# Kernel optimization log

Hardware: AMD Instinct MI355X
Metric: run time of the kernel (lower is better)

The kernel has to match this reference:

```python
import jax, jax.numpy as jnp
import numpy as np

D = 128
N_DRUG = 100000
N_PROT = 50000
E_DD, E_DP, E_PD = 800000, 600000, 600000
EPS = 1e-5


def setup_inputs() -> dict:
    key = jax.random.key(0)
    ks = jax.random.split(key, 19)
    f32 = jnp.float32
    return {
        "x_drug": jax.random.normal(ks[0], (N_DRUG, D), f32),
        "x_prot": jax.random.normal(ks[1], (N_PROT, D), f32),
        "Wagg_dd": jax.random.normal(ks[2], (D, D), f32) * 0.05,
        "Wagg_dp": jax.random.normal(ks[3], (D, D), f32) * 0.05,
        "Wagg_pd": jax.random.normal(ks[4], (D, D), f32) * 0.05,
        "W_drug": jax.random.normal(ks[5], (D, 2 * D), f32) * 0.05,
        "b_drug": jax.random.normal(ks[6], (D,), f32) * 0.01,
        "W_prot": jax.random.normal(ks[7], (D, 2 * D), f32) * 0.05,
        "b_prot": jax.random.normal(ks[8], (D,), f32) * 0.01,
        "g_drug": jnp.ones((D,), f32),
        "be_drug": jnp.zeros((D,), f32),
        "g_prot": jnp.ones((D,), f32),
        "be_prot": jnp.zeros((D,), f32),
        "ei_dd_src": jax.random.randint(ks[9], (E_DD,), 0, N_DRUG, jnp.int64 if jax.config.jax_enable_x64 else jnp.int32),
        "ei_dd_dst": jax.random.randint(ks[10], (E_DD,), 0, N_DRUG),
        "ei_dp_src": jax.random.randint(ks[11], (E_DP,), 0, N_DRUG),
        "ei_dp_dst": jax.random.randint(ks[12], (E_DP,), 0, N_PROT),
        "ei_pd_src": jax.random.randint(ks[13], (E_PD,), 0, N_PROT),
        "ei_pd_dst": jax.random.randint(ks[14], (E_PD,), 0, N_DRUG),
    }


def _rel_agg(x_src, W_agg, src_idx, dst_idx, n_dst):
    # gather -> per-relation Linear (no bias) + ReLU -> scatter-mean
    h = jax.nn.relu(x_src[src_idx] @ W_agg.T)            # [E, D]
    s = jax.ops.segment_sum(h, dst_idx, num_segments=n_dst)
    c = jax.ops.segment_sum(jnp.ones((src_idx.shape[0],), h.dtype), dst_idx, num_segments=n_dst)
    return s / jnp.maximum(c, 1.0)[:, None]


def _layernorm(x, g, b):
    mu = jnp.mean(x, axis=-1, keepdims=True)
    var = jnp.mean(jnp.square(x - mu), axis=-1, keepdims=True)
    return (x - mu) * jax.lax.rsqrt(var + EPS) * g + b


def _node_update(h_self, h_agg, W, b, g, be):
    h = jax.nn.relu(jnp.concatenate([h_self, h_agg], axis=-1) @ W.T + b)
    return _layernorm(h + h_self, g, be)  # dropout is identity in eval


def reference(x_drug, x_prot, Wagg_dd, Wagg_dp, Wagg_pd, W_drug, b_drug,
              W_prot, b_prot, g_drug, be_drug, g_prot, be_prot,
              ei_dd_src, ei_dd_dst, ei_dp_src, ei_dp_dst, ei_pd_src, ei_pd_dst):
    agg_dd = _rel_agg(x_drug, Wagg_dd, ei_dd_src, ei_dd_dst, N_DRUG)
    agg_pd = _rel_agg(x_prot, Wagg_pd, ei_pd_src, ei_pd_dst, N_DRUG)
    agg_drug = (agg_dd + agg_pd) * 0.5                   # mean over relations into 'drug'
    agg_prot = _rel_agg(x_drug, Wagg_dp, ei_dp_src, ei_dp_dst, N_PROT)
    out_drug = _node_update(x_drug, agg_drug, W_drug, b_drug, g_drug, be_drug)
    out_prot = _node_update(x_prot, agg_prot, W_prot, b_prot, g_prot, be_prot)
    # pack the per-type outputs into one array [N_DRUG + N_PROT, D]
    return jnp.concatenate([out_drug, out_prot], axis=0)
```

## Files before the change

kernel.cpp:

```cpp
#include <hip/hip_runtime.h>

#define D 128
#define ND 100000
#define NP 50000
#define NE_DD 800000
#define NE_DP 600000
#define NE_PD 600000
#define NE_TOT 2000000

#define NTOT 250000
#define NBC 490
#define NC 250880
#define CHUNKA 4096
#define NBLKA 489
#define CHUNKIT 16
#define SEGCAP 8192

#define TF_BD 1563
#define TF_BP 391
#define NU_BD 782
#define NU_BP 391

typedef __bf16 bf16;
typedef __attribute__((ext_vector_type(8))) __bf16 bf16x8;
typedef __attribute__((ext_vector_type(2))) __bf16 bf16x2;
typedef __attribute__((ext_vector_type(4))) float f32x4;
typedef __attribute__((ext_vector_type(2))) float f32x2;

#define OFF_WDD   0UL
#define OFF_WDP   32768UL
#define OFF_WPD   65536UL
#define OFF_WDRUG 98304UL
#define OFF_WPROT 163840UL
#define OFF_YDD   229376UL
#define OFF_YDP   (OFF_YDD + 25600000UL)
#define OFF_YPD   (OFF_YDP + 25600000UL)
#define OFF_AGGD  (OFF_YPD + 12800000UL)
#define OFF_AGGP  (OFF_AGGD + 25600000UL)
#define OFF_BCNT  (OFF_AGGP + 12800000UL)
#define OFF_GCUR  (OFF_BCNT + 2048UL)
#define OFF_CBASE (OFF_GCUR + 2048UL)
#define OFF_RP    (OFF_CBASE + 2048UL)
#define OFF_PAIRS (OFF_RP + 1003520UL)
#define OFF_POOL  (OFF_PAIRS + 16000000UL)

__device__ __forceinline__ unsigned enc1(float f)
{
    unsigned t = __float_as_uint(f * 0x1p-120f);
    t = (t + 0x80000u) >> 20;
    return t > 0x7Eu ? 0x7Eu : t;
}
__device__ __forceinline__ unsigned enc4(float a, float b, float c, float d)
{
    return enc1(a) | (enc1(b) << 8) | (enc1(c) << 16) | (enc1(d) << 24);
}

__global__ __launch_bounds__(256) void prep_kernel(
    const float* __restrict__ w0, const float* __restrict__ w1,
    const float* __restrict__ w2, const float* __restrict__ w3,
    const float* __restrict__ w4,
    bf16* __restrict__ o0, bf16* __restrict__ o1, bf16* __restrict__ o2,
    bf16* __restrict__ o3, bf16* __restrict__ o4,
    const int* __restrict__ dd_dst, const int* __restrict__ pd_dst,
    const int* __restrict__ dp_dst, int* __restrict__ bcnt)
{
    int m = blockIdx.y;
    int t = threadIdx.x;
    if (m == 5) {
        __shared__ int h[NBC];
        for (int i = t; i < NBC; i += 256) h[i] = 0;
        __syncthreads();
        for (int e = blockIdx.x * 256 + t; e < NE_TOT; e += 128 * 256) {
            int didx;
            if (e < NE_DD) didx = dd_dst[e];
            else if (e < NE_DD + NE_PD) didx = ND + pd_dst[e - NE_DD];
            else didx = 2 * ND + dp_dst[e - NE_DD - NE_PD];
            atomicAdd(&h[didx >> 9], 1);
        }
        __syncthreads();
        for (int i = t; i < NBC; i += 256)
            if (h[i]) atomicAdd(&bcnt[i], h[i]);
        return;
    }
    int i = blockIdx.x * 256 + t;
    const float* src; bf16* dst; int n; bool perm;
    switch (m) {
        case 0: src = w0; dst = o0; n = D * D; perm = false; break;
        case 1: src = w1; dst = o1; n = D * D; perm = false; break;
        case 2: src = w2; dst = o2; n = D * D; perm = false; break;
        case 3: src = w3; dst = o3; n = D * 2 * D; perm = true; break;
        default: src = w4; dst = o4; n = D * 2 * D; perm = true; break;
    }
    if (i < n) {
        int si = i;
        if (perm) {
            int col = i & 255;
            if (col >= 128) {
                int p = col - 128;
                si = (i & ~255) | (128 + (p & 7) * 16 + (p >> 3));
            }
        }
        dst[i] = (bf16)src[si];
    }
}

__global__ __launch_bounds__(256) void scan_kernel(
    const int* __restrict__ bcnt, int* __restrict__ cbase, int* __restrict__ gcur)
{
    __shared__ int ps[256];
    int t = threadIdx.x;
    int i0 = 2 * t, i1 = 2 * t + 1;
    int c0 = (i0 < NBC) ? bcnt[i0] : 0;
    int c1 = (i1 < NBC) ? bcnt[i1] : 0;
    ps[t] = c0 + c1;
    __syncthreads();
#pragma unroll
    for (int off = 1; off < 256; off <<= 1) {
        int add = (t >= off) ? ps[t - off] : 0;
        __syncthreads();
        ps[t] += add;
        __syncthreads();
    }
    int excl = ps[t] - (c0 + c1);
    if (i0 <= NBC) cbase[i0] = excl;
    if (i0 < NBC) gcur[i0] = excl;
    if (i1 < NBC) { cbase[i1] = excl + c0; gcur[i1] = excl + c0; }
}

__device__ __forceinline__ bf16x8 load_a_f32(const float* __restrict__ xr)
{
    float4 f0 = *(const float4*)xr;
    float4 f1 = *(const float4*)(xr + 4);
    bf16x8 a;
    a[0] = (bf16)f0.x; a[1] = (bf16)f0.y; a[2] = (bf16)f0.z; a[3] = (bf16)f0.w;
    a[4] = (bf16)f1.x; a[5] = (bf16)f1.y; a[6] = (bf16)f1.z; a[7] = (bf16)f1.w;
    return a;
}

__device__ __forceinline__ void transform_drug(
    const float* __restrict__ x, const bf16* __restrict__ W1,
    const bf16* __restrict__ W2, unsigned char* __restrict__ y1,
    unsigned char* __restrict__ y2, int blk)
{
    int lane = threadIdx.x & 63;
    int wave = threadIdx.x >> 6;
    int q = lane >> 4, c = lane & 15;
    int mb = blk * 64 + wave * 16;

    f32x4 acc1[8], acc2[8];
#pragma unroll
    for (int nt = 0; nt < 8; nt++) { acc1[nt] = 0; acc2[nt] = 0; }

    int rowA = min(mb + c, ND - 1);
#pragma unroll
    for (int kb = 0; kb < 4; kb++) {
        int k = kb * 32 + q * 8;
        bf16x8 a = load_a_f32(x + (long)rowA * D + k);
#pragma unroll
        for (int nt = 0; nt < 8; nt++) {
            bf16x8 b1 = *(const bf16x8*)(W1 + (nt * 16 + c) * D + k);
            bf16x8 b2 = *(const bf16x8*)(W2 + (nt * 16 + c) * D + k);
            acc1[nt] = __builtin_amdgcn_mfma_f32_16x16x32_bf16(a, b1, acc1[nt], 0, 0, 0);
            acc2[nt] = __builtin_amdgcn_mfma_f32_16x16x32_bf16(a, b2, acc2[nt], 0, 0, 0);
        }
    }
#pragma unroll
    for (int r = 0; r < 4; r++) {
        int row = mb + q * 4 + r;
        if (row < ND) {
            float v1[8], v2[8];
#pragma unroll
            for (int nt = 0; nt < 8; nt++) {
                v1[nt] = fmaxf(acc1[nt][r], 0.f);
                v2[nt] = fmaxf(acc2[nt][r], 0.f);
            }
            uint2 p1, p2;
            p1.x = enc4(v1[0], v1[1], v1[2], v1[3]);
            p1.y = enc4(v1[4], v1[5], v1[6], v1[7]);
            p2.x = enc4(v2[0], v2[1], v2[2], v2[3]);
            p2.y = enc4(v2[4], v2[5], v2[6], v2[7]);
            *(uint2*)(y1 + (long)row * D + c * 8) = p1;
            *(uint2*)(y2 + (long)row * D + c * 8) = p2;
        }
    }
}

__device__ __forceinline__ void transform_prot(
    const float* __restrict__ x, const bf16* __restrict__ W1,
    unsigned char* __restrict__ y1, int blk)
{
    int lane = threadIdx.x & 63;
    int wave = threadIdx.x >> 6;
    int q = lane >> 4, c = lane & 15;
    int mb = blk * 128 + wave * 32;

    f32x4 acc[2][8];
#pragma unroll
    for (int mt = 0; mt < 2; mt++)
#pragma unroll
        for (int nt = 0; nt < 8; nt++) acc[mt][nt] = 0;

#pragma unroll
    for (int kb = 0; kb < 4; kb++) {
        int k = kb * 32 + q * 8;
        bf16x8 a[2];
#pragma unroll
        for (int mt = 0; mt < 2; mt++) {
            int row = min(mb + mt * 16 + c, NP - 1);
            a[mt] = load_a_f32(x + (long)row * D + k);
        }
#pragma unroll
        for (int nt = 0; nt < 8; nt++) {
            bf16x8 b1 = *(const bf16x8*)(W1 + (nt * 16 + c) * D + k);
#pragma unroll
            for (int mt = 0; mt < 2; mt++)
                acc[mt][nt] = __builtin_amdgcn_mfma_f32_16x16x32_bf16(a[mt], b1, acc[mt][nt], 0, 0, 0);
        }
    }
#pragma unroll
    for (int mt = 0; mt < 2; mt++)
#pragma unroll
        for (int r = 0; r < 4; r++) {
            int row = mb + mt * 16 + q * 4 + r;
            if (row < NP) {
                float v[8];
#pragma unroll
                for (int nt = 0; nt < 8; nt++)
                    v[nt] = fmaxf(acc[mt][nt][r], 0.f);
                uint2 p1;
                p1.x = enc4(v[0], v[1], v[2], v[3]);
                p1.y = enc4(v[4], v[5], v[6], v[7]);
                *(uint2*)(y1 + (long)row * D + c * 8) = p1;
            }
        }
}

__global__ __launch_bounds__(256) void transform_kernel(
    const float* __restrict__ x_drug, const float* __restrict__ x_prot,
    const bf16* __restrict__ Wdd, const bf16* __restrict__ Wdp,
    const bf16* __restrict__ Wpd,
    unsigned char* __restrict__ y_dd, unsigned char* __restrict__ y_dp,
    unsigned char* __restrict__ y_pd)
{
    int blk = blockIdx.x;
    if (blk < TF_BD)
        transform_drug(x_drug, Wdd, Wdp, y_dd, y_dp, blk);
    else
        transform_prot(x_prot, Wpd, y_pd, blk - TF_BD);
}

__global__ __launch_bounds__(256) void binA_kernel(
    const int* __restrict__ dd_src, const int* __restrict__ dd_dst,
    const int* __restrict__ pd_src, const int* __restrict__ pd_dst,
    const int* __restrict__ dp_src, const int* __restrict__ dp_dst,
    int* __restrict__ gcur, unsigned* __restrict__ pairs)
{
    __shared__ int h[NBC];
    __shared__ int gb[NBC];
    __shared__ int2 pr[CHUNKA];
    __shared__ unsigned short rk[CHUNKA];
    for (int i = threadIdx.x; i < NBC; i += 256) h[i] = 0;
    __syncthreads();
    int base = blockIdx.x * CHUNKA;
    for (int it = 0; it < CHUNKIT; it++) {
        int idx = it * 256 + threadIdx.x;
        int e = base + idx;
        int didx = -1, sv = 0;
        if (e < NE_TOT) {
            if (e < NE_DD) { didx = dd_dst[e]; sv = dd_src[e]; }
            else if (e < NE_DD + NE_PD) { int u = e - NE_DD; didx = ND + pd_dst[u]; sv = pd_src[u]; }
            else { int u = e - NE_DD - NE_PD; didx = 2 * ND + dp_dst[u]; sv = dp_src[u]; }
            rk[idx] = (unsigned short)atomicAdd(&h[didx >> 9], 1);
        }
        pr[idx] = make_int2(didx, sv);
    }
    __syncthreads();
    for (int b = threadIdx.x; b < NBC; b += 256) {
        int c = h[b];
        gb[b] = c ? atomicAdd(&gcur[b], c) : 0;
    }
    __syncthreads();
    for (int it = 0; it < CHUNKIT; it++) {
        int idx = it * 256 + threadIdx.x;
        int2 p = pr[idx];
        if (p.x >= 0)
            pairs[gb[p.x >> 9] + rk[idx]] =
                ((unsigned)(p.x & 511) << 17) | (unsigned)p.y;
    }
}

__global__ __launch_bounds__(256) void sortB_kernel(
    const int* __restrict__ cbase, const unsigned* __restrict__ pairs,
    int* __restrict__ pool, int* __restrict__ rp)
{
    __shared__ int h[512];
    __shared__ int excl[512];
    __shared__ int ps[256];
    __shared__ unsigned short rk[SEGCAP];
    __shared__ int outl[SEGCAP];

    int b = blockIdx.x;
    int s0 = cbase[b], s1 = cbase[b + 1];
    int n = s1 - s0;
    if (n > SEGCAP) n = SEGCAP;
    int t = threadIdx.x;
    h[t] = 0; h[t + 256] = 0;
    __syncthreads();

    for (int i = t; i < n; i += 256) {
        unsigned p = pairs[s0 + i];
        rk[i] = (unsigned short)atomicAdd(&h[p >> 17], 1);
    }
    __syncthreads();

    int c0 = h[2 * t], c1 = h[2 * t + 1];
    ps[t] = c0 + c1;
    __syncthreads();
#pragma unroll
    for (int off = 1; off < 256; off <<= 1) {
        int add = (t >= off) ? ps[t - off] : 0;
        __syncthreads();
        ps[t] += add;
        __syncthreads();
    }
    int pe = ps[t] - (c0 + c1);
    excl[2 * t] = pe;
    excl[2 * t + 1] = pe + c0;
    __syncthreads();

    int nb = b * 512;
    rp[nb + 2 * t] = s0 + excl[2 * t];
    rp[nb + 2 * t + 1] = s0 + excl[2 * t + 1];

    for (int i = t; i < n; i += 256) {
        unsigned p = pairs[s0 + i];
        outl[excl[p >> 17] + rk[i]] = (int)(p & 0x1FFFFu);
    }
    __syncthreads();
    for (int i = t; i < n; i += 256)
        pool[s0 + i] = outl[i];
}

__device__ __forceinline__ void accw(unsigned short w, f32x2* acc)
{
    float lo = __uint_as_float((unsigned)(w & 0xFFu) << 20);
    float hi = __uint_as_float((unsigned)(w >> 8) << 20);
    acc->x = fmaf(lo, 0x1p120f, acc->x);
    acc->y = fmaf(hi, 0x1p120f, acc->y);
}

__device__ __forceinline__ void acc_seg(
    const int* __restrict__ pool, int s, int e,
    const unsigned short* __restrict__ y, int lane, f32x2* acc)
{
    for (int base = s; base < e; base += 64) {
        int cnt = e - base;
        if (cnt > 64) cnt = 64;
        int idxv = pool[base + min(lane, cnt - 1)];
        int t = 0;
        for (; t + 4 <= cnt; t += 4) {
            int s0 = __builtin_amdgcn_readlane(idxv, t);
            int s1 = __builtin_amdgcn_readlane(idxv, t + 1);
            int s2 = __builtin_amdgcn_readlane(idxv, t + 2);
            int s3 = __builtin_amdgcn_readlane(idxv, t + 3);
            unsigned short w0 = y[(long)s0 * 64 + lane];
            unsigned short w1 = y[(long)s1 * 64 + lane];
            unsigned short w2 = y[(long)s2 * 64 + lane];
            unsigned short w3 = y[(long)s3 * 64 + lane];
            accw(w0, acc); accw(w1, acc); accw(w2, acc); accw(w3, acc);
        }
        for (; t < cnt; t++) {
            int sid = __builtin_amdgcn_readlane(idxv, t);
            accw(y[(long)sid * 64 + lane], acc);
        }
    }
}

__global__ __launch_bounds__(256) void gather_kernel(
    const int* __restrict__ rp, const int* __restrict__ pool,
    const unsigned short* __restrict__ y_dd,
    const unsigned short* __restrict__ y_pd,
    const unsigned short* __restrict__ y_dp,
    bf16* __restrict__ agg_d, bf16* __restrict__ agg_p)
{
    int wid = blockIdx.x * 4 + (threadIdx.x >> 6);
    int lane = threadIdx.x & 63;

    if (wid < ND) {
        int g = wid;
        int s1 = rp[g], e1 = rp[g + 1];
        int s2 = rp[ND + g], e2 = rp[ND + g + 1];
        f32x2 a; a.x = 0.f; a.y = 0.f;
        f32x2 b; b.x = 0.f; b.y = 0.f;
        acc_seg(pool, s1, e1, y_dd, lane, &a);
        acc_seg(pool, s2, e2, y_pd, lane, &b);
        float i1 = 0.5f / (float)max(e1 - s1, 1);
        float i2 = 0.5f / (float)max(e2 - s2, 1);
        f32x2 r = a * i1 + b * i2;
        bf16x2 o; o[0] = (bf16)r.x; o[1] = (bf16)r.y;
        *(bf16x2*)(agg_d + (long)g * D + lane * 2) = o;
    } else if (wid < ND + NP) {
        int p = wid - ND;
        int s1 = rp[2 * ND + p], e1 = rp[2 * ND + p + 1];
        f32x2 a; a.x = 0.f; a.y = 0.f;
        acc_seg(pool, s1, e1, y_dp, lane, &a);
        float i1 = 1.0f / (float)max(e1 - s1, 1);
        f32x2 r = a * i1;
        bf16x2 o; o[0] = (bf16)r.x; o[1] = (bf16)r.y;
        *(bf16x2*)(agg_p + (long)p * D + lane * 2) = o;
    }
}

__device__ __forceinline__ void node_update_body(
    const float* __restrict__ x, const bf16* __restrict__ agg,
    const bf16* __restrict__ W, const float* __restrict__ b,
    const float* __restrict__ g, const float* __restrict__ be,
    float* __restrict__ out, int M, int blk)
{
    int lane = threadIdx.x & 63;
    int wave = threadIdx.x >> 6;
    int q = lane >> 4, c = lane & 15;
    int mb = blk * 128 + wave * 32;

    f32x4 acc[2][8];
#pragma unroll
    for (int mt = 0; mt < 2; mt++)
#pragma unroll
        for (int nt = 0; nt < 8; nt++) acc[mt][nt] = 0;

#pragma unroll
    for (int kb = 0; kb < 8; kb++) {
        bf16x8 a[2];
#pragma unroll
        for (int mt = 0; mt < 2; mt++) {
            int row = min(mb + mt * 16 + c, M - 1);
            if (kb < 4)
                a[mt] = load_a_f32(x + (long)row * D + kb * 32 + q * 8);
            else
                a[mt] = *(const bf16x8*)(agg + (long)row * D + (kb - 4) * 32 + q * 8);
        }
#pragma unroll
        for (int nt = 0; nt < 8; nt++) {
            bf16x8 bw = *(const bf16x8*)(W + (nt * 16 + c) * (2 * D) + kb * 32 + q * 8);
#pragma unroll
            for (int mt = 0; mt < 2; mt++)
                acc[mt][nt] = __builtin_amdgcn_mfma_f32_16x16x32_bf16(a[mt], bw, acc[mt][nt], 0, 0, 0);
        }
    }

    float bv[8], gv[8], bev[8];
#pragma unroll
    for (int nt = 0; nt < 8; nt++) {
        int col = nt * 16 + c;
        bv[nt] = b[col]; gv[nt] = g[col]; bev[nt] = be[col];
    }
#pragma unroll
    for (int mt = 0; mt < 2; mt++)
#pragma unroll
        for (int r = 0; r < 4; r++) {
            int row = mb + mt * 16 + q * 4 + r;
            int rowc = min(row, M - 1);
            const float* xr = x + (long)rowc * D + c;
            float v[8];
            float sum = 0.f, sq = 0.f;
#pragma unroll
            for (int nt = 0; nt < 8; nt++) {
                float h = fmaxf(acc[mt][nt][r] + bv[nt], 0.f);
                float t = h + xr[nt * 16];
                v[nt] = t; sum += t; sq += t * t;
            }
#pragma unroll
            for (int m = 1; m < 16; m <<= 1) {
                sum += __shfl_xor(sum, m, 64);
                sq  += __shfl_xor(sq,  m, 64);
            }
            float mu   = sum * (1.f / 128.f);
            float var  = sq  * (1.f / 128.f) - mu * mu;
            float rstd = rsqrtf(var + 1e-5f);
            if (row < M) {
                float* op = out + (long)row * D + c;
#pragma unroll
                for (int nt = 0; nt < 8; nt++)
                    op[nt * 16] = (v[nt] - mu) * rstd * gv[nt] + bev[nt];
            }
        }
}

__global__ __launch_bounds__(256) void node_update_kernel(
    const float* __restrict__ x_drug, const float* __restrict__ x_prot,
    const bf16* __restrict__ agg_d, const bf16* __restrict__ agg_p,
    const bf16* __restrict__ Wdrug, const float* __restrict__ b_drug,
    const float* __restrict__ g_drug, const float* __restrict__ be_drug,
    const bf16* __restrict__ Wprot, const float* __restrict__ b_prot,
    const float* __restrict__ g_prot, const float* __restrict__ be_prot,
    float* __restrict__ out)
{
    int blk = blockIdx.x;
    if (blk < NU_BD)
        node_update_body(x_drug, agg_d, Wdrug, b_drug, g_drug, be_drug,
                         out, ND, blk);
    else
        node_update_body(x_prot, agg_p, Wprot, b_prot, g_prot, be_prot,
                         out + (long)ND * D, NP, blk - NU_BD);
}

extern "C" void kernel_launch(void* const* d_in, const int* in_sizes, int n_in,
                              void* d_out, int out_size, void* d_ws, size_t ws_size,
                              hipStream_t stream)
{
    const float* x_drug  = (const float*)d_in[0];
    const float* x_prot  = (const float*)d_in[1];
    const float* Wagg_dd = (const float*)d_in[2];
    const float* Wagg_dp = (const float*)d_in[3];
    const float* Wagg_pd = (const float*)d_in[4];
    const float* W_drug  = (const float*)d_in[5];
    const float* b_drug  = (const float*)d_in[6];
    const float* W_prot  = (const float*)d_in[7];
    const float* b_prot  = (const float*)d_in[8];
    const float* g_drug  = (const float*)d_in[9];
    const float* be_drug = (const float*)d_in[10];
    const float* g_prot  = (const float*)d_in[11];
    const float* be_prot = (const float*)d_in[12];
    const int* dd_src = (const int*)d_in[13];
    const int* dd_dst = (const int*)d_in[14];
    const int* dp_src = (const int*)d_in[15];
    const int* dp_dst = (const int*)d_in[16];
    const int* pd_src = (const int*)d_in[17];
    const int* pd_dst = (const int*)d_in[18];

    char* ws = (char*)d_ws;
    bf16* Wdd   = (bf16*)(ws + OFF_WDD);
    bf16* Wdp   = (bf16*)(ws + OFF_WDP);
    bf16* Wpd   = (bf16*)(ws + OFF_WPD);
    bf16* Wdrug = (bf16*)(ws + OFF_WDRUG);
    bf16* Wprot = (bf16*)(ws + OFF_WPROT);
    unsigned char* y_dd = (unsigned char*)(ws + OFF_YDD);
    unsigned char* y_dp = (unsigned char*)(ws + OFF_YDP);
    unsigned char* y_pd = (unsigned char*)(ws + OFF_YPD);
    bf16* agg_d = (bf16*)(ws + OFF_AGGD);
    bf16* agg_p = (bf16*)(ws + OFF_AGGP);
    int* bcnt   = (int*)(ws + OFF_BCNT);
    int* gcur   = (int*)(ws + OFF_GCUR);
    int* cbase  = (int*)(ws + OFF_CBASE);
    int* rp     = (int*)(ws + OFF_RP);
    unsigned* pairs = (unsigned*)(ws + OFF_PAIRS);
    int* pool   = (int*)(ws + OFF_POOL);
    float* out  = (float*)d_out;

    hipMemsetAsync(bcnt, 0, NBC * sizeof(int), stream);

    prep_kernel<<<dim3(128, 6), 256, 0, stream>>>(
        Wagg_dd, Wagg_dp, Wagg_pd, W_drug, W_prot,
        Wdd, Wdp, Wpd, Wdrug, Wprot,
        dd_dst, pd_dst, dp_dst, bcnt);

    scan_kernel<<<1, 256, 0, stream>>>(bcnt, cbase, gcur);

    binA_kernel<<<NBLKA, 256, 0, stream>>>(
        dd_src, dd_dst, pd_src, pd_dst, dp_src, dp_dst, gcur, pairs);

    sortB_kernel<<<NBC, 256, 0, stream>>>(cbase, pairs, pool, rp);

    transform_kernel<<<TF_BD + TF_BP, 256, 0, stream>>>(
        x_drug, x_prot, Wdd, Wdp, Wpd, y_dd, y_dp, y_pd);

    gather_kernel<<<(ND + NP + 3) / 4, 256, 0, stream>>>(
        rp, pool, (const unsigned short*)y_dd, (const unsigned short*)y_pd,
        (const unsigned short*)y_dp, agg_d, agg_p);

    node_update_kernel<<<NU_BD + NU_BP, 256, 0, stream>>>(
        x_drug, x_prot, agg_d, agg_p,
        Wdrug, b_drug, g_drug, be_drug,
        Wprot, b_prot, g_prot, be_prot, out);
}
```

Measured before the change: 435.0 us.

## Fuse gather with node update via LDS staging and enlarge transform row tiles

Merges the segment-mean gather kernel into the node-update kernel. Each block now aggregates its 128 nodes into a padded LDS buffer, then runs the MFMA GEMM and LayerNorm reading the aggregate from LDS instead of a global bf16 array. This removes the agg_d/agg_p global round trip and one launch. The cost is less latency-hiding parallelism in the gather phase, since each wave handles 32 nodes serially and the LDS use limits occupancy. The transform kernel also doubles the rows per wave so weight loads are reused across more MFMAs, at the price of more registers; launch bounds are set to allow 2 blocks per CU.

Result: slower. 511.0 us (+17.5%).

```diff
diff --git a/kernel.cpp b/kernel.cpp
--- a/kernel.cpp
+++ b/kernel.cpp
@@ -16,10 +16,12 @@
 #define CHUNKIT 16
 #define SEGCAP 8192
 
-#define TF_BD 1563
-#define TF_BP 391
+#define TF_BD 782
+#define TF_BP 196
 #define NU_BD 782
 #define NU_BP 391
+
+#define AGG_STRIDE 272
 
 typedef __bf16 bf16;
 typedef __attribute__((ext_vector_type(8))) __bf16 bf16x8;
@@ -35,9 +37,7 @@
 #define OFF_YDD   229376UL
 #define OFF_YDP   (OFF_YDD + 25600000UL)
 #define OFF_YPD   (OFF_YDP + 25600000UL)
-#define OFF_AGGD  (OFF_YPD + 12800000UL)
-#define OFF_AGGP  (OFF_AGGD + 25600000UL)
-#define OFF_BCNT  (OFF_AGGP + 12800000UL)
+#define OFF_BCNT  (OFF_YPD + 12800000UL)
 #define OFF_GCUR  (OFF_BCNT + 2048UL)
 #define OFF_CBASE (OFF_GCUR + 2048UL)
 #define OFF_RP    (OFF_CBASE + 2048UL)
@@ -145,44 +145,55 @@
     int lane = threadIdx.x & 63;
     int wave = threadIdx.x >> 6;
     int q = lane >> 4, c = lane & 15;
-    int mb = blk * 64 + wave * 16;
-
-    f32x4 acc1[8], acc2[8];
-#pragma unroll
-    for (int nt = 0; nt < 8; nt++) { acc1[nt] = 0; acc2[nt] = 0; }
-
-    int rowA = min(mb + c, ND - 1);
+    int mb = blk * 128 + wave * 32;
+
+    f32x4 acc1[2][8], acc2[2][8];
+#pragma unroll
+    for (int mt = 0; mt < 2; mt++)
+#pragma unroll
+        for (int nt = 0; nt < 8; nt++) { acc1[mt][nt] = 0; acc2[mt][nt] = 0; }
+
 #pragma unroll
     for (int kb = 0; kb < 4; kb++) {
         int k = kb * 32 + q * 8;
-        bf16x8 a = load_a_f32(x + (long)rowA * D + k);
+        bf16x8 a[2];
+#pragma unroll
+        for (int mt = 0; mt < 2; mt++) {
+            int row = min(mb + mt * 16 + c, ND - 1);
+            a[mt] = load_a_f32(x + (long)row * D + k);
+        }
 #pragma unroll
         for (int nt = 0; nt < 8; nt++) {
             bf16x8 b1 = *(const bf16x8*)(W1 + (nt * 16 + c) * D + k);
             bf16x8 b2 = *(const bf16x8*)(W2 + (nt * 16 + c) * D + k);
-            acc1[nt] = __builtin_amdgcn_mfma_f32_16x16x32_bf16(a, b1, acc1[nt], 0, 0, 0);
-            acc2[nt] = __builtin_amdgcn_mfma_f32_16x16x32_bf16(a, b2, acc2[nt], 0, 0, 0);
-        }
-    }
-#pragma unroll
-    for (int r = 0; r < 4; r++) {
-        int row = mb + q * 4 + r;
-        if (row < ND) {
-            float v1[8], v2[8];
-#pragma unroll
-            for (int nt = 0; nt < 8; nt++) {
-                v1[nt] = fmaxf(acc1[nt][r], 0.f);
-                v2[nt] = fmaxf(acc2[nt][r], 0.f);
-            }
-            uint2 p1, p2;
-            p1.x = enc4(v1[0], v1[1], v1[2], v1[3]);
-            p1.y = enc4(v1[4], v1[5], v1[6], v1[7]);
-            p2.x = enc4(v2[0], v2[1], v2[2], v2[3]);
-            p2.y = enc4(v2[4], v2[5], v2[6], v2[7]);
-            *(uint2*)(y1 + (long)row * D + c * 8) = p1;
-            *(uint2*)(y2 + (long)row * D + c * 8) = p2;
-        }
-    }
+#pragma unroll
+            for (int mt = 0; mt < 2; mt++) {
+                acc1[mt][nt] = __builtin_amdgcn_mfma_f32_16x16x32_bf16(a[mt], b1, acc1[mt][nt], 0, 0, 0);
+                acc2[mt][nt] = __builtin_amdgcn_mfma_f32_16x16x32_bf16(a[mt], b2, acc2[mt][nt], 0, 0, 0);
+            }
+        }
+    }
+#pragma unroll
+    for (int mt = 0; mt < 2; mt++)
+#pragma unroll
+        for (int r = 0; r < 4; r++) {
+            int row = mb + mt * 16 + q * 4 + r;
+            if (row < ND) {
+                float v1[8], v2[8];
+#pragma unroll
+                for (int nt = 0; nt < 8; nt++) {
+                    v1[nt] = fmaxf(acc1[mt][nt][r], 0.f);
+                    v2[nt] = fmaxf(acc2[mt][nt][r], 0.f);
+                }
+                uint2 p1, p2;
+                p1.x = enc4(v1[0], v1[1], v1[2], v1[3]);
+                p1.y = enc4(v1[4], v1[5], v1[6], v1[7]);
+                p2.x = enc4(v2[0], v2[1], v2[2], v2[3]);
+                p2.y = enc4(v2[4], v2[5], v2[6], v2[7]);
+                *(uint2*)(y1 + (long)row * D + c * 8) = p1;
+                *(uint2*)(y2 + (long)row * D + c * 8) = p2;
+            }
+        }
 }
 
 __device__ __forceinline__ void transform_prot(
@@ -192,20 +203,20 @@
     int lane = threadIdx.x & 63;
     int wave = threadIdx.x >> 6;
     int q = lane >> 4, c = lane & 15;
-    int mb = blk * 128 + wave * 32;
-
-    f32x4 acc[2][8];
-#pragma unroll
-    for (int mt = 0; mt < 2; mt++)
+    int mb = blk * 256 + wave * 64;
+
+    f32x4 acc[4][8];
+#pragma unroll
+    for (int mt = 0; mt < 4; mt++)
 #pragma unroll
         for (int nt = 0; nt < 8; nt++) acc[mt][nt] = 0;
 
 #pragma unroll
     for (int kb = 0; kb < 4; kb++) {
         int k = kb * 32 + q * 8;
-        bf16x8 a[2];
-#pragma unroll
-        for (int mt = 0; mt < 2; mt++) {
+        bf16x8 a[4];
+#pragma unroll
+        for (int mt = 0; mt < 4; mt++) {
             int row = min(mb + mt * 16 + c, NP - 1);
             a[mt] = load_a_f32(x + (long)row * D + k);
         }
@@ -213,12 +224,12 @@
         for (int nt = 0; nt < 8; nt++) {
             bf16x8 b1 = *(const bf16x8*)(W1 + (nt * 16 + c) * D + k);
 #pragma unroll
-            for (int mt = 0; mt < 2; mt++)
+            for (int mt = 0; mt < 4; mt++)
                 acc[mt][nt] = __builtin_amdgcn_mfma_f32_16x16x32_bf16(a[mt], b1, acc[mt][nt], 0, 0, 0);
         }
     }
 #pragma unroll
-    for (int mt = 0; mt < 2; mt++)
+    for (int mt = 0; mt < 4; mt++)
 #pragma unroll
         for (int r = 0; r < 4; r++) {
             int row = mb + mt * 16 + q * 4 + r;
@@ -235,7 +246,7 @@
         }
 }
 
-__global__ __launch_bounds__(256) void transform_kernel(
+__global__ __launch_bounds__(256, 2) void transform_kernel(
     const float* __restrict__ x_drug, const float* __restrict__ x_prot,
     const bf16* __restrict__ Wdd, const bf16* __restrict__ Wdp,
     const bf16* __restrict__ Wpd,
@@ -376,132 +387,125 @@
     }
 }
 
-__global__ __launch_bounds__(256) void gather_kernel(
+__global__ __launch_bounds__(256, 2) void fused_gnu_kernel(
     const int* __restrict__ rp, const int* __restrict__ pool,
     const unsigned short* __restrict__ y_dd,
     const unsigned short* __restrict__ y_pd,
     const unsigned short* __restrict__ y_dp,
-    bf16* __restrict__ agg_d, bf16* __restrict__ agg_p)
-{
-    int wid = blockIdx.x * 4 + (threadIdx.x >> 6);
-    int lane = threadIdx.x & 63;
-
-    if (wid < ND) {
-        int g = wid;
-        int s1 = rp[g], e1 = rp[g + 1];
-        int s2 = rp[ND + g], e2 = rp[ND + g + 1];
-        f32x2 a; a.x = 0.f; a.y = 0.f;
-        f32x2 b; b.x = 0.f; b.y = 0.f;
-        acc_seg(pool, s1, e1, y_dd, lane, &a);
-        acc_seg(pool, s2, e2, y_pd, lane, &b);
-        float i1 = 0.5f / (float)max(e1 - s1, 1);
-        float i2 = 0.5f / (float)max(e2 - s2, 1);
-        f32x2 r = a * i1 + b * i2;
-        bf16x2 o; o[0] = (bf16)r.x; o[1] = (bf16)r.y;
-        *(bf16x2*)(agg_d + (long)g * D + lane * 2) = o;
-    } else if (wid < ND + NP) {
-        int p = wid - ND;
-        int s1 = rp[2 * ND + p], e1 = rp[2 * ND + p + 1];
-        f32x2 a; a.x = 0.f; a.y = 0.f;
-        acc_seg(pool, s1, e1, y_dp, lane, &a);
-        float i1 = 1.0f / (float)max(e1 - s1, 1);
-        f32x2 r = a * i1;
-        bf16x2 o; o[0] = (bf16)r.x; o[1] = (bf16)r.y;
-        *(bf16x2*)(agg_p + (long)p * D + lane * 2) = o;
-    }
-}
-
-__device__ __forceinline__ void node_update_body(
-    const float* __restrict__ x, const bf16* __restrict__ agg,
-    const bf16* __restrict__ W, const float* __restrict__ b,
-    const float* __restrict__ g, const float* __restrict__ be,
-    float* __restrict__ out, int M, int blk)
-{
-    int lane = threadIdx.x & 63;
-    int wave = threadIdx.x >> 6;
-    int q = lane >> 4, c = lane & 15;
-    int mb = blk * 128 + wave * 32;
-
-    f32x4 acc[2][8];
-#pragma unroll
-    for (int mt = 0; mt < 2; mt++)
-#pragma unroll
-        for (int nt = 0; nt < 8; nt++) acc[mt][nt] = 0;
-
-#pragma unroll
-    for (int kb = 0; kb < 8; kb++) {
-        bf16x8 a[2];
-#pragma unroll
-        for (int mt = 0; mt < 2; mt++) {
-            int row = min(mb + mt * 16 + c, M - 1);
-            if (kb < 4)
-                a[mt] = load_a_f32(x + (long)row * D + kb * 32 + q * 8);
-            else
-                a[mt] = *(const bf16x8*)(agg + (long)row * D + (kb - 4) * 32 + q * 8);
-        }
-#pragma unroll
-        for (int nt = 0; nt < 8; nt++) {
-            bf16x8 bw = *(const bf16x8*)(W + (nt * 16 + c) * (2 * D) + kb * 32 + q * 8);
-#pragma unroll
-            for (int mt = 0; mt < 2; mt++)
-                acc[mt][nt] = __builtin_amdgcn_mfma_f32_16x16x32_bf16(a[mt], bw, acc[mt][nt], 0, 0, 0);
-        }
-    }
-
-    float bv[8], gv[8], bev[8];
-#pragma unroll
-    for (int nt = 0; nt < 8; nt++) {
-        int col = nt * 16 + c;
-        bv[nt] = b[col]; gv[nt] = g[col]; bev[nt] = be[col];
-    }
-#pragma unroll
-    for (int mt = 0; mt < 2; mt++)
-#pragma unroll
-        for (int r = 0; r < 4; r++) {
-            int row = mb + mt * 16 + q * 4 + r;
-            int rowc = min(row, M - 1);
-            const float* xr = x + (long)rowc * D + c;
-            float v[8];
-            float sum = 0.f, sq = 0.f;
-#pragma unroll
-            for (int nt = 0; nt < 8; nt++) {
-                float h = fmaxf(acc[mt][nt][r] + bv[nt], 0.f);
-                float t = h + xr[nt * 16];
-                v[nt] = t; sum += t; sq += t * t;
-            }
-#pragma unroll
-            for (int m = 1; m < 16; m <<= 1) {
-                sum += __shfl_xor(sum, m, 64);
-                sq  += __shfl_xor(sq,  m, 64);
-            }
-            float mu   = sum * (1.f / 128.f);
-            float var  = sq  * (1.f / 128.f) - mu * mu;
-            float rstd = rsqrtf(var + 1e-5f);
-            if (row < M) {
-                float* op = out + (long)row * D + c;
-#pragma unroll
-                for (int nt = 0; nt < 8; nt++)
-                    op[nt * 16] = (v[nt] - mu) * rstd * gv[nt] + bev[nt];
-            }
-        }
-}
-
-__global__ __launch_bounds__(256) void node_update_kernel(
     const float* __restrict__ x_drug, const float* __restrict__ x_prot,
-    const bf16* __restrict__ agg_d, const bf16* __restrict__ agg_p,
     const bf16* __restrict__ Wdrug, const float* __restrict__ b_drug,
     const float* __restrict__ g_drug, const float* __restrict__ be_drug,
     const bf16* __restrict__ Wprot, const float* __restrict__ b_prot,
     const float* __restrict__ g_prot, const float* __restrict__ be_prot,
     float* __restrict__ out)
 {
+    __shared__ unsigned char ldsagg[128 * AGG_STRIDE];
+
     int blk = blockIdx.x;
-    if (blk < NU_BD)
-        node_update_body(x_drug, agg_d, Wdrug, b_drug, g_drug, be_drug,
-                         out, ND, blk);
-    else
-        node_update_body(x_prot, agg_p, Wprot, b_prot, g_prot, be_prot,
-                         out + (long)ND * D, NP, blk - NU_BD);
+    int wave = threadIdx.x >> 6;
+    int lane = threadIdx.x & 63;
+    bool isD = blk < NU_BD;
+    int mb = (isD ? blk : blk - NU_BD) * 128;
+    int M = isD ? ND : NP;
+
+    for (int i = 0; i < 32; i++) {
+        int node = mb + wave * 32 + i;
+        if (node < M) {
+            f32x2 r;
+            if (isD) {
+                int s1 = rp[node], e1 = rp[node + 1];
+                int s2 = rp[ND + node], e2 = rp[ND + node + 1];
+                f32x2 a; a.x = 0.f; a.y = 0.f;
+                f32x2 b2; b2.x = 0.f; b2.y = 0.f;
+                acc_seg(pool, s1, e1, y_dd, lane, &a);
+                acc_seg(pool, s2, e2, y_pd, lane, &b2);
+                float i1 = 0.5f / (float)max(e1 - s1, 1);
+                float i2 = 0.5f / (float)max(e2 - s2, 1);
+                r = a * i1 + b2 * i2;
+            } else {
+                int s1 = rp[2 * ND + node], e1 = rp[2 * ND + node + 1];
+                f32x2 a; a.x = 0.f; a.y = 0.f;
+                acc_seg(pool, s1, e1, y_dp, lane, &a);
+                r = a * (1.0f / (float)max(e1 - s1, 1));
+            }
+            bf16x2 o; o[0] = (bf16)r.x; o[1] = (bf16)r.y;
+            *(bf16x2*)(ldsagg + (wave * 32 + i) * AGG_STRIDE + lane * 4) = o;
+        }
+    }
+    __syncthreads();
+
+    const float* x  = isD ? x_drug : x_prot;
+    const bf16* W   = isD ? Wdrug : Wprot;
+    const float* b  = isD ? b_drug : b_prot;
+    const float* g  = isD ? g_drug : g_prot;
+    const float* be = isD ? be_drug : be_prot;
+    float* o        = isD ? out : out + (long)ND * D;
+
+    int q = lane >> 4, c = lane & 15;
+    int lcap = M - 1 - mb;
+
+    f32x4 acc[2][8];
+#pragma unroll
+    for (int mt = 0; mt < 2; mt++)
+#pragma unroll
+        for (int nt = 0; nt < 8; nt++) acc[mt][nt] = 0;
+
+#pragma unroll
+    for (int kb = 0; kb < 8; kb++) {
+        bf16x8 a[2];
+#pragma unroll
+        for (int mt = 0; mt < 2; mt++) {
+            int lr = min(wave * 32 + mt * 16 + c, lcap);
+            if (kb < 4)
+                a[mt] = load_a_f32(x + (long)(mb + lr) * D + kb * 32 + q * 8);
+            else
+                a[mt] = *(const bf16x8*)(ldsagg + lr * AGG_STRIDE + (kb - 4) * 64 + q * 16);
+        }
+#pragma unroll
+        for (int nt = 0; nt < 8; nt++) {
+            bf16x8 bw = *(const bf16x8*)(W + (nt * 16 + c) * (2 * D) + kb * 32 + q * 8);
+#pragma unroll
+            for (int mt = 0; mt < 2; mt++)
+                acc[mt][nt] = __builtin_amdgcn_mfma_f32_16x16x32_bf16(a[mt], bw, acc[mt][nt], 0, 0, 0);
+        }
+    }
+
+    float bv[8], gv[8], bev[8];
+#pragma unroll
+    for (int nt = 0; nt < 8; nt++) {
+        int col = nt * 16 + c;
+        bv[nt] = b[col]; gv[nt] = g[col]; bev[nt] = be[col];
+    }
+#pragma unroll
+    for (int mt = 0; mt < 2; mt++)
+#pragma unroll
+        for (int r = 0; r < 4; r++) {
+            int row = mb + wave * 32 + mt * 16 + q * 4 + r;
+            int rowc = min(row, M - 1);
+            const float* xr = x + (long)rowc * D + c;
+            float v[8];
+            float sum = 0.f, sq = 0.f;
+#pragma unroll
+            for (int nt = 0; nt < 8; nt++) {
+                float h = fmaxf(acc[mt][nt][r] + bv[nt], 0.f);
+                float t = h + xr[nt * 16];
+                v[nt] = t; sum += t; sq += t * t;
+            }
+#pragma unroll
+            for (int m = 1; m < 16; m <<= 1) {
+                sum += __shfl_xor(sum, m, 64);
+                sq  += __shfl_xor(sq,  m, 64);
+            }
+            float mu   = sum * (1.f / 128.f);
+            float var  = sq  * (1.f / 128.f) - mu * mu;
+            float rstd = rsqrtf(var + 1e-5f);
+            if (row < M) {
+                float* op = o + (long)row * D + c;
+#pragma unroll
+                for (int nt = 0; nt < 8; nt++)
+                    op[nt * 16] = (v[nt] - mu) * rstd * gv[nt] + bev[nt];
+            }
+        }
 }
 
 extern "C" void kernel_launch(void* const* d_in, const int* in_sizes, int n_in,
@@ -537,8 +541,6 @@
     unsigned char* y_dd = (unsigned char*)(ws + OFF_YDD);
     unsigned char* y_dp = (unsigned char*)(ws + OFF_YDP);
     unsigned char* y_pd = (unsigned char*)(ws + OFF_YPD);
-    bf16* agg_d = (bf16*)(ws + OFF_AGGD);
-    bf16* agg_p = (bf16*)(ws + OFF_AGGP);
     int* bcnt   = (int*)(ws + OFF_BCNT);
     int* gcur   = (int*)(ws + OFF_GCUR);
     int* cbase  = (int*)(ws + OFF_CBASE);
@@ -564,12 +566,11 @@
     transform_kernel<<<TF_BD + TF_BP, 256, 0, stream>>>(
         x_drug, x_prot, Wdd, Wdp, Wpd, y_dd, y_dp, y_pd);
 
-    gather_kernel<<<(ND + NP + 3) / 4, 256, 0, stream>>>(
-        rp, pool, (const unsigned short*)y_dd, (const unsigned short*)y_pd,
-        (const unsigned short*)y_dp, agg_d, agg_p);
-
-    node_update_kernel<<<NU_BD + NU_BP, 256, 0, stream>>>(
-        x_drug, x_prot, agg_d, agg_p,
+    fused_gnu_kernel<<<NU_BD + NU_BP, 256, 0, stream>>>(
+        rp, pool,
+        (const unsigned short*)y_dd, (const unsigned short*)y_pd,
+        (const unsigned short*)y_dp,
+        x_drug, x_prot,
         Wdrug, b_drug, g_drug, be_drug,
         Wprot, b_prot, g_prot, be_prot, out);
 }
```
